# Kernel tuning notes

Hardware: AMD Instinct MI355X
Metric: run time of the kernel (lower is better)

Reference implementation:

```python
import jax, jax.numpy as jnp
import numpy as np

B, T, C, K, V = 4, 4096, 128, 64, 64
EPS = 1e-5


def layer_norm(x, g, b):
    mu = jnp.mean(x, axis=-1, keepdims=True)
    var = jnp.var(x, axis=-1, keepdims=True)
    return (x - mu) * jax.lax.rsqrt(var + EPS) * g + b


def setup_inputs() -> dict:
    key = jax.random.key(0)
    ks = jax.random.split(key, 8)
    s = 1.0 / np.sqrt(C)
    return {
        "x": jax.random.normal(ks[0], (B, T, C), dtype=jnp.float32),
        "Wq": jax.random.uniform(ks[1], (C, K), jnp.float32, -s, s),
        "bq": jnp.zeros((K,), jnp.float32),
        "Wk": jax.random.uniform(ks[2], (C, K), jnp.float32, -s, s),
        "bk": jnp.zeros((K,), jnp.float32),
        "Wv": jax.random.uniform(ks[3], (C, V), jnp.float32, -s, s),
        "bv": jnp.zeros((V,), jnp.float32),
        "gq": jnp.ones((K,), jnp.float32), "bgq": jnp.zeros((K,), jnp.float32),
        "gk": jnp.ones((K,), jnp.float32), "bgk": jnp.zeros((K,), jnp.float32),
        "gv": jnp.ones((V,), jnp.float32), "bgv": jnp.zeros((V,), jnp.float32),
        "go": jnp.ones((V,), jnp.float32), "bgo": jnp.zeros((V,), jnp.float32),
    }


def reference(x, Wq, bq, Wk, bk, Wv, bv, gq, bgq, gk, bgk, gv, bgv, go, bgo):
    # projections: B x T x {K,K,V}
    q = layer_norm(x @ Wq + bq, gq, bgq)
    k = layer_norm(x @ Wk + bk, gk, bgk)
    v = layer_norm(x @ Wv + bv, gv, bgv)
    sqrt_k = jnp.asarray(np.sqrt(K), x.dtype)
    # full B x T x T causal score matrix (faithful to the original bmm+mask)
    logits = jnp.einsum("btk,bsk->bts", q, k) / sqrt_k
    t = jnp.arange(T)
    causal = t[:, None] >= t[None, :]  # lower-triangular incl. diagonal
    logits = jnp.where(causal[None], logits, -jnp.inf)
    probs = jax.nn.softmax(logits, axis=-1)
    read = jnp.einsum("bts,bsv->btv", probs, v)
    read = layer_norm(read, go, bgo)
    return jnp.concatenate([x, read], axis=2)  # B x T x (C+V)
```

## Files before the change

### kernel.cpp

```cpp
#include <hip/hip_runtime.h>

#define TT 4096

typedef unsigned short u16;
typedef unsigned int u32;

typedef short bf16x8 __attribute__((ext_vector_type(8)));
typedef float f32x4 __attribute__((ext_vector_type(4)));

union U8 {
  uint2 q[2];
  uint4 u4;
  bf16x8 v;
  short s[8];
  u32 w[4];
};

static __device__ __forceinline__ u16 f2bf(float f) {
  union { float f; u32 u; } cv;
  cv.f = f;
  u32 r = cv.u + 0x7FFFu + ((cv.u >> 16) & 1u);
  return (u16)(r >> 16);
}
static __device__ __forceinline__ u32 pk2(float a, float b) {
  return (u32)f2bf(a) | ((u32)f2bf(b) << 16);
}
static __device__ __forceinline__ float bf2f(u16 h) {
  union { u32 u; float f; } cv;
  cv.u = ((u32)h) << 16;
  return cv.f;
}
static __device__ __forceinline__ float exp2a(float x) {
  float r; asm("v_exp_f32 %0, %1" : "=v"(r) : "v"(x)); return r;
}
static __device__ __forceinline__ u32 cvtpk(float lo, float hi) {
  u32 r; asm("v_cvt_pk_bf16_f32 %0, %1, %2" : "=v"(r) : "v"(lo), "v"(hi)); return r;
}

__global__ __launch_bounds__(64)
void wpack(const float* __restrict__ Wq, const float* __restrict__ Wk,
           const float* __restrict__ Wv, u16* __restrict__ wf)
{
  const int g = blockIdx.x;
  const int p = g >> 4, s = (g >> 2) & 3, nt = g & 3;
  const int l = threadIdx.x, lg = l >> 4, l15 = l & 15;
  const float* W = (p == 0) ? Wq : (p == 1) ? Wk : Wv;
  const int n = l15 + 16 * nt;
  U8 o;
#pragma unroll
  for (int j = 0; j < 8; ++j) {
    int k = 32 * s + ((j < 4) ? (4 * lg + j) : (16 + 4 * lg + (j - 4)));
    o.s[j] = (short)f2bf(W[k * 64 + n]);
  }
  *(uint4*)(wf + (size_t)(g * 64 + l) * 8) = o.u4;
}

__global__ __launch_bounds__(256)
void proj_mfma(const float* __restrict__ x, const u16* __restrict__ wf,
               const float* __restrict__ bq, const float* __restrict__ bk,
               const float* __restrict__ bv,
               const float* __restrict__ gq, const float* __restrict__ bgq,
               const float* __restrict__ gk, const float* __restrict__ bgk,
               const float* __restrict__ gv, const float* __restrict__ bgv,
               u16* __restrict__ qo, u16* __restrict__ ko, u16* __restrict__ vto,
               float* __restrict__ out)
{
  __shared__ u16 xs[64 * 130];
  const int bx = blockIdx.x;
  const int xcd = bx & 7, i = bx >> 3;
  const int tile = xcd * 32 + (i & 31);
  const int p = i >> 5;
  const int rowbase = tile * 64;
  const int t = threadIdx.x;

  {
    const int row = t >> 2, seg = t & 3;
    const float4* src = (const float4*)(x + (size_t)(rowbase + row) * 128 + seg * 32);
    float4 f[8];
#pragma unroll
    for (int q = 0; q < 8; ++q) f[q] = src[q];
    if ((p == 0 && seg < 2) || (p == 1 && seg >= 2)) {
      float4* dst = (float4*)(out + (size_t)(rowbase + row) * 192 + seg * 32);
#pragma unroll
      for (int q = 0; q < 8; ++q) dst[q] = f[q];
    }
    const int base = row * 256 + seg * 64;
    const int swz = (row & 7) << 4;
    char* xb = (char*)xs;
#pragma unroll
    for (int q = 0; q < 4; ++q) {
      uint4 u;
      u.x = pk2(f[2 * q].x, f[2 * q].y);
      u.y = pk2(f[2 * q].z, f[2 * q].w);
      u.z = pk2(f[2 * q + 1].x, f[2 * q + 1].y);
      u.w = pk2(f[2 * q + 1].z, f[2 * q + 1].w);
      *(uint4*)(xb + ((base + 16 * q) ^ swz)) = u;
    }
  }

  const int w = t >> 6, l = t & 63, lg = l >> 4, l15 = l & 15;
  U8 bfr[4][4];
  const u16* wp = wf + (size_t)p * (16 * 64 * 8);
#pragma unroll
  for (int s = 0; s < 4; ++s)
#pragma unroll
    for (int nt = 0; nt < 4; ++nt)
      bfr[s][nt].u4 = *(const uint4*)(wp + ((s * 4 + nt) * 64 + l) * 8);

  __syncthreads();

  f32x4 acc[4];
#pragma unroll
  for (int nt = 0; nt < 4; ++nt) acc[nt] = (f32x4){0.f, 0.f, 0.f, 0.f};
  const int abase = (16 * w + l15) * 256;
  const int aswz = (l15 & 7) << 4;
  const char* xb = (const char*)xs;
#pragma unroll
  for (int s = 0; s < 4; ++s) {
    U8 af;
    af.q[0] = *(const uint2*)(xb + ((abase + s * 64 + 8 * lg) ^ aswz));
    af.q[1] = *(const uint2*)(xb + ((abase + s * 64 + 8 * lg + 32) ^ aswz));
#pragma unroll
    for (int nt = 0; nt < 4; ++nt)
      acc[nt] = __builtin_amdgcn_mfma_f32_16x16x32_bf16(af.v, bfr[s][nt].v, acc[nt], 0, 0, 0);
  }

  const float* bb = (p == 0) ? bq : (p == 1) ? bk : bv;
  const float* gg = (p == 0) ? gq : (p == 1) ? gk : gv;
  const float* hh = (p == 0) ? bgq : (p == 1) ? bgk : bgv;
  float bcol[4], gcol[4], hcol[4];
#pragma unroll
  for (int nt = 0; nt < 4; ++nt) {
    int col = l15 + 16 * nt;
    bcol[nt] = bb[col]; gcol[nt] = gg[col]; hcol[nt] = hh[col];
  }
  float vals[4][4];
#pragma unroll
  for (int nt = 0; nt < 4; ++nt)
#pragma unroll
    for (int r = 0; r < 4; ++r) vals[nt][r] = acc[nt][r] + bcol[nt];

  float s1[4], s2[4];
#pragma unroll
  for (int r = 0; r < 4; ++r) {
    s1[r] = vals[0][r] + vals[1][r] + vals[2][r] + vals[3][r];
    s2[r] = vals[0][r] * vals[0][r] + vals[1][r] * vals[1][r]
          + vals[2][r] * vals[2][r] + vals[3][r] * vals[3][r];
#pragma unroll
    for (int d = 1; d < 16; d <<= 1) {
      s1[r] += __shfl_xor(s1[r], d);
      s2[r] += __shfl_xor(s2[r], d);
    }
  }

  if (p < 2) {
    u16* dst = (p == 0) ? qo : ko;
#pragma unroll
    for (int r = 0; r < 4; ++r) {
      float mu = s1[r] * (1.f / 64.f);
      float var = s2[r] * (1.f / 64.f) - mu * mu;
      float rs = rsqrtf(var + 1e-5f);
      int grow = rowbase + 16 * w + 4 * lg + r;
#pragma unroll
      for (int nt = 0; nt < 4; ++nt)
        dst[(size_t)grow * 64 + l15 + 16 * nt] =
            f2bf((vals[nt][r] - mu) * rs * gcol[nt] + hcol[nt]);
    }
  } else {
    u16* vls = xs;
    __syncthreads();
#pragma unroll
    for (int r = 0; r < 4; ++r) {
      float mu = s1[r] * (1.f / 64.f);
      float var = s2[r] * (1.f / 64.f) - mu * mu;
      float rs = rsqrtf(var + 1e-5f);
      int row = 16 * w + 4 * lg + r;
#pragma unroll
      for (int nt = 0; nt < 4; ++nt)
        vls[row * 65 + l15 + 16 * nt] =
            f2bf((vals[nt][r] - mu) * rs * gcol[nt] + hcol[nt]);
    }
    __syncthreads();
    const int b = rowbase >> 12;
    const int tl = rowbase & 4095;
    const int col = t >> 2;
    const int tq = (t & 3) * 16;
    U8 o0, o1;
#pragma unroll
    for (int i = 0; i < 8; ++i) o0.s[i] = (short)vls[(tq + i) * 65 + col];
#pragma unroll
    for (int i = 0; i < 8; ++i) o1.s[i] = (short)vls[(tq + 8 + i) * 65 + col];
    u16* dst = vto + (size_t)(b * 64 + col) * TT + tl + tq;
    *(uint4*)(dst + 0) = o0.u4;
    *(uint4*)(dst + 8) = o1.u4;
  }
}

__global__ __launch_bounds__(256)
void attn_pair4n(const u16* __restrict__ qg, const u16* __restrict__ kg,
                 const u16* __restrict__ vtg,
                 float* __restrict__ lP, u16* __restrict__ aP)
{
  __shared__ u16 kl4[4 * 64 * 64];
  __shared__ u16 vl4[4 * 64 * 64];
  const int bx = blockIdx.x;
  const int xcd = bx & 7, b = xcd >> 1, e2 = xcd & 1;
  const int j = e2 * 136 + (bx >> 3);
  int M = 0;
  while ((M + 1) * (M + 2) <= j) ++M;
  const int ip = j - M * (M + 1);
  const int e = (ip >= M + 1) ? 1 : 0;
  const int s = ip - e * (M + 1);
  const int pr = 2 * M + e;
  const int qa = 2 * pr, qb = 2 * pr + 1;
  const int it0 = 4 * s;
  const int it1 = min(it0 + 4, qb + 1);

  const int t = threadIdx.x;
  const int w = t >> 6, l = t & 63;
  const int l15 = l & 15, lg = l >> 4;
  const int swzl = (l15 & 7) << 4;

  const int wbaseA = qa * 64 + 16 * w, wbaseB = qb * 64 + 16 * w;
  const int qrowA = wbaseA + l15, qrowB = wbaseB + l15;
  const u16* qrpA = qg + (size_t)(b * TT + qrowA) * 64;
  const u16* qrpB = qg + (size_t)(b * TT + qrowB) * 64;
  U8 qfA[2], qfB[2];
#pragma unroll
  for (int hh = 0; hh < 2; ++hh) {
    qfA[hh].q[0] = *(const uint2*)(qrpA + 32 * hh + 4 * lg);
    qfA[hh].q[1] = *(const uint2*)(qrpA + 32 * hh + 4 * lg + 16);
    qfB[hh].q[0] = *(const uint2*)(qrpB + 32 * hh + 4 * lg);
    qfB[hh].q[1] = *(const uint2*)(qrpB + 32 * hh + 4 * lg + 16);
  }

  {
    const int key = t >> 2, part = t & 3;
    const int sbase = key * 128 + part * 32;
    const int ssw = (key & 7) << 4;
    uint4 kr[4][2], vr[4][2];
#pragma unroll
    for (int tt = 0; tt < 4; ++tt) {
      int tile = it0 + tt; if (tile >= it1) tile = it1 - 1;
      const u16* ks = kg + (size_t)(b * TT + tile * 64 + key) * 64 + part * 16;
      kr[tt][0] = ((const uint4*)ks)[0];
      kr[tt][1] = ((const uint4*)ks)[1];
      const u16* vs = vtg + (size_t)(b * 64 + key) * TT + tile * 64 + part * 16;
      vr[tt][0] = ((const uint4*)vs)[0];
      vr[tt][1] = ((const uint4*)vs)[1];
    }
#pragma unroll
    for (int tt = 0; tt < 4; ++tt) {
      char* kd = (char*)kl4 + tt * 8192;
      char* vd = (char*)vl4 + tt * 8192;
      *(uint4*)(kd + ((sbase + 0) ^ ssw)) = kr[tt][0];
      *(uint4*)(kd + ((sbase + 16) ^ ssw)) = kr[tt][1];
      *(uint4*)(vd + ((sbase + 0) ^ ssw)) = vr[tt][0];
      *(uint4*)(vd + ((sbase + 16) ^ ssw)) = vr[tt][1];
    }
  }
  __syncthreads();

  const float C = 0.18033688011112042f;
  float lA = 0.f, lB = 0.f;
  f32x4 accA[4], accB[4];
#pragma unroll
  for (int ct = 0; ct < 4; ++ct) {
    accA[ct] = (f32x4){0.f, 0.f, 0.f, 0.f};
    accB[ct] = (f32x4){0.f, 0.f, 0.f, 0.f};
  }

  int toff = 0;
  for (int it = it0; it < it1; ++it, toff += 8192) {
    const int kb = it * 64;
    const char* kp = (const char*)kl4 + toff;
    const char* vp = (const char*)vl4 + toff;

    f32x4 stA[4], stB[4];
    __builtin_amdgcn_s_setprio(1);
#pragma unroll
    for (int t4 = 0; t4 < 4; ++t4) {
      const int rbase = (16 * t4 + l15) * 128 + 8 * lg;
      U8 kf0, kf1;
      kf0.q[0] = *(const uint2*)(kp + ((rbase + 0) ^ swzl));
      kf0.q[1] = *(const uint2*)(kp + ((rbase + 32) ^ swzl));
      kf1.q[0] = *(const uint2*)(kp + ((rbase + 64) ^ swzl));
      kf1.q[1] = *(const uint2*)(kp + ((rbase + 96) ^ swzl));
      f32x4 dA = {0.f, 0.f, 0.f, 0.f};
      dA = __builtin_amdgcn_mfma_f32_16x16x32_bf16(kf0.v, qfA[0].v, dA, 0, 0, 0);
      dA = __builtin_amdgcn_mfma_f32_16x16x32_bf16(kf1.v, qfA[1].v, dA, 0, 0, 0);
      stA[t4] = dA;
      f32x4 dB = {0.f, 0.f, 0.f, 0.f};
      dB = __builtin_amdgcn_mfma_f32_16x16x32_bf16(kf0.v, qfB[0].v, dB, 0, 0, 0);
      dB = __builtin_amdgcn_mfma_f32_16x16x32_bf16(kf1.v, qfB[1].v, dB, 0, 0, 0);
      stB[t4] = dB;
    }
    __builtin_amdgcn_s_setprio(0);

    float pA[16], pB[16];
    const bool maskA = (kb + 63 > wbaseA);
    if (maskA) {
#pragma unroll
      for (int t4 = 0; t4 < 4; ++t4) {
#pragma unroll
        for (int r = 0; r < 4; ++r) {
          int keyidx = kb + 16 * t4 + 4 * lg + r;
          float e = exp2a(stA[t4][r] * C);
          pA[t4 * 4 + r] = (keyidx > qrowA) ? 0.f : e;
        }
      }
    } else {
#pragma unroll
      for (int t4 = 0; t4 < 4; ++t4) {
#pragma unroll
        for (int r = 0; r < 4; ++r) pA[t4 * 4 + r] = exp2a(stA[t4][r] * C);
      }
    }
    const bool maskB = (kb + 63 > wbaseB);
    if (maskB) {
#pragma unroll
      for (int t4 = 0; t4 < 4; ++t4) {
#pragma unroll
        for (int r = 0; r < 4; ++r) {
          int keyidx = kb + 16 * t4 + 4 * lg + r;
          float e = exp2a(stB[t4][r] * C);
          pB[t4 * 4 + r] = (keyidx > qrowB) ? 0.f : e;
        }
      }
    } else {
#pragma unroll
      for (int t4 = 0; t4 < 4; ++t4) {
#pragma unroll
        for (int r = 0; r < 4; ++r) pB[t4 * 4 + r] = exp2a(stB[t4][r] * C);
      }
    }
    float smA[8], smB[8];
#pragma unroll
    for (int i = 0; i < 8; ++i) {
      smA[i] = pA[2 * i] + pA[2 * i + 1];
      smB[i] = pB[2 * i] + pB[2 * i + 1];
    }
#pragma unroll
    for (int i = 0; i < 4; ++i) {
      smA[i] = smA[2 * i] + smA[2 * i + 1];
      smB[i] = smB[2 * i] + smB[2 * i + 1];
    }
    float rsA = (smA[0] + smA[1]) + (smA[2] + smA[3]);
    float rsB = (smB[0] + smB[1]) + (smB[2] + smB[3]);
    rsA += __shfl_xor(rsA, 16);
    rsB += __shfl_xor(rsB, 16);
    rsA += __shfl_xor(rsA, 32);
    rsB += __shfl_xor(rsB, 32);
    lA += rsA;
    lB += rsB;

    U8 paA[2], paB[2];
#pragma unroll
    for (int u = 0; u < 2; ++u) {
#pragma unroll
      for (int k2 = 0; k2 < 4; ++k2) {
        paA[u].w[k2] = cvtpk(pA[8 * u + 2 * k2], pA[8 * u + 2 * k2 + 1]);
        paB[u].w[k2] = cvtpk(pB[8 * u + 2 * k2], pB[8 * u + 2 * k2 + 1]);
      }
    }

    __builtin_amdgcn_s_setprio(1);
#pragma unroll
    for (int ct = 0; ct < 4; ++ct) {
      const int vb = (16 * ct + l15) * 128 + 8 * lg;
#pragma unroll
      for (int u = 0; u < 2; ++u) {
        U8 vf;
        vf.q[0] = *(const uint2*)(vp + ((vb + 64 * u + 0) ^ swzl));
        vf.q[1] = *(const uint2*)(vp + ((vb + 64 * u + 32) ^ swzl));
        accA[ct] = __builtin_amdgcn_mfma_f32_16x16x32_bf16(paA[u].v, vf.v, accA[ct], 0, 0, 0);
        accB[ct] = __builtin_amdgcn_mfma_f32_16x16x32_bf16(paB[u].v, vf.v, accB[ct], 0, 0, 0);
      }
    }
    __builtin_amdgcn_s_setprio(0);
  }

  const int jqA = 2 * M * (M + 1) + (2 * e) * (M + 1) + s;
  const int jqB = 2 * M * (M + 1) + (2 * e + 1) * (M + 1) + s;
  const size_t pbA = (size_t)(b * 544 + jqA) * 64;
  const size_t pbB = (size_t)(b * 544 + jqB) * 64;
  if (lg == 0) {
    lP[pbA + 16 * w + l15] = lA;
    lP[pbB + 16 * w + l15] = lB;
  }
#pragma unroll
  for (int ct = 0; ct < 4; ++ct) {
#pragma unroll
    for (int r = 0; r < 4; ++r) {
      int rin = 16 * w + 4 * lg + r;
      aP[(pbA + rin) * 64 + l15 + 16 * ct] = f2bf(accA[ct][r]);
      aP[(pbB + rin) * 64 + l15 + 16 * ct] = f2bf(accB[ct][r]);
    }
  }
}

__global__ __launch_bounds__(256)
void attn_merge4n(const float* __restrict__ lP, const u16* __restrict__ aP,
                  const float* __restrict__ go, const float* __restrict__ bgo,
                  float* __restrict__ out)
{
  const int t = threadIdx.x;
  const int w = t >> 6, c = t & 63;
  const int row = blockIdx.x * 4 + w;
  const int tid2 = row >> 6, rin = row & 63;
  const int b = tid2 >> 6, q = tid2 & 63;
  const int Q = q >> 2;
  const int base_q = b * 544 + 2 * Q * (Q + 1) + (q & 3) * (Q + 1);
  const int ns = Q + 1;

  float L = 0.f, o = 0.f;
  for (int s = 0; s < ns; ++s) {
    const size_t pb = (size_t)(base_q + s) * 64;
    L += lP[pb + rin];
    o += bf2f(aP[(pb + rin) * 64 + c]);
  }
  o /= L;

  float s1 = o, s2 = o * o;
#pragma unroll
  for (int d = 1; d < 64; d <<= 1) {
    s1 += __shfl_xor(s1, d);
    s2 += __shfl_xor(s2, d);
  }
  float mu = s1 * (1.f / 64.f);
  float var = s2 * (1.f / 64.f) - mu * mu;
  float rs = rsqrtf(var + 1e-5f);
  out[(size_t)row * 192 + 128 + c] = (o - mu) * rs * go[c] + bgo[c];
}

__global__ __launch_bounds__(128)
void attn1(const u16* __restrict__ qg, const u16* __restrict__ kg,
           const u16* __restrict__ vtg,
           const float* __restrict__ go, const float* __restrict__ bgo,
           float* __restrict__ out)
{
  __shared__ u16 kl[64 * 64];
  __shared__ u16 vl[64 * 64];
  const int bx = blockIdx.x;
  const int tt = (bx < 256) ? bx : (767 - bx);
  const int b = tt >> 7;
  const int q0 = (tt & 127) * 32;
  const int tid = threadIdx.x;
  const int w = tid >> 6;
  const int l = tid & 63;
  const int l15 = l & 15;
  const int lg = l >> 4;
  const int swzl = (l15 & 7) << 4;

  const int qrow = q0 + 16 * w + l15;
  const u16* qrp = qg + (size_t)(b * TT + qrow) * 64;
  U8 qf[2];
#pragma unroll
  for (int h = 0; h < 2; ++h) {
    qf[h].q[0] = *(const uint2*)(qrp + 32 * h + 4 * lg);
    qf[h].q[1] = *(const uint2*)(qrp + 32 * h + 4 * lg + 16);
  }

  float m_run = -1e30f, l_run = 0.f;
  f32x4 acc[4];
#pragma unroll
  for (int ct = 0; ct < 4; ++ct) acc[ct] = (f32x4){0.f, 0.f, 0.f, 0.f};

  const int nkv = (q0 >> 6) + 1;
  for (int it = 0; it < nkv; ++it) {
    const int kb = it * 64;
    {
      const int key = tid >> 1;
      const int dh = (tid & 1) * 32;
      const u16* ks = kg + (size_t)(b * TT + kb + key) * 64 + dh;
      uint4 d0 = *(const uint4*)(ks + 0);
      uint4 d1 = *(const uint4*)(ks + 8);
      uint4 d2 = *(const uint4*)(ks + 16);
      uint4 d3 = *(const uint4*)(ks + 24);
      const int base = key * 128 + dh * 2;
      const int sw = (key & 7) << 4;
      char* kd = (char*)kl;
      *(uint4*)(kd + ((base + 0) ^ sw)) = d0;
      *(uint4*)(kd + ((base + 16) ^ sw)) = d1;
      *(uint4*)(kd + ((base + 32) ^ sw)) = d2;
      *(uint4*)(kd + ((base + 48) ^ sw)) = d3;
      const u16* vs = vtg + (size_t)(b * 64 + key) * TT + kb + dh;
      uint4 e0 = *(const uint4*)(vs + 0);
      uint4 e1 = *(const uint4*)(vs + 8);
      uint4 e2 = *(const uint4*)(vs + 16);
      uint4 e3 = *(const uint4*)(vs + 24);
      char* vd = (char*)vl;
      *(uint4*)(vd + ((base + 0) ^ sw)) = e0;
      *(uint4*)(vd + ((base + 16) ^ sw)) = e1;
      *(uint4*)(vd + ((base + 32) ^ sw)) = e2;
      *(uint4*)(vd + ((base + 48) ^ sw)) = e3;
    }
    __syncthreads();

    f32x4 st[4];
#pragma unroll
    for (int t4 = 0; t4 < 4; ++t4) {
      const int rbase = (16 * t4 + l15) * 128 + 8 * lg;
      const char* kp = (const char*)kl;
      U8 kf0, kf1;
      kf0.q[0] = *(const uint2*)(kp + ((rbase + 0) ^ swzl));
      kf0.q[1] = *(const uint2*)(kp + ((rbase + 32) ^ swzl));
      kf1.q[0] = *(const uint2*)(kp + ((rbase + 64) ^ swzl));
      kf1.q[1] = *(const uint2*)(kp + ((rbase + 96) ^ swzl));
      f32x4 d = {0.f, 0.f, 0.f, 0.f};
      d = __builtin_amdgcn_mfma_f32_16x16x32_bf16(kf0.v, qf[0].v, d, 0, 0, 0);
      d = __builtin_amdgcn_mfma_f32_16x16x32_bf16(kf1.v, qf[1].v, d, 0, 0, 0);
      st[t4] = d;
    }

    float sv[16];
    const bool needmask = (kb + 63 > q0 + 16 * w);
#pragma unroll
    for (int t4 = 0; t4 < 4; ++t4) {
#pragma unroll
      for (int r = 0; r < 4; ++r) {
        float sc = st[t4][r] * 0.125f;
        if (needmask) {
          int keyidx = kb + 16 * t4 + 4 * lg + r;
          if (keyidx > qrow) sc = -1e30f;
        }
        sv[t4 * 4 + r] = sc;
      }
    }
    float mt = sv[0];
#pragma unroll
    for (int i = 1; i < 16; ++i) mt = fmaxf(mt, sv[i]);
    mt = fmaxf(mt, __shfl_xor(mt, 16));
    mt = fmaxf(mt, __shfl_xor(mt, 32));
    const float mnew = fmaxf(m_run, mt);
    const float al = __expf(m_run - mnew);
    float p[16];
    float rsum = 0.f;
#pragma unroll
    for (int i = 0; i < 16; ++i) { p[i] = __expf(sv[i] - mnew); rsum += p[i]; }
    rsum += __shfl_xor(rsum, 16);
    rsum += __shfl_xor(rsum, 32);
    l_run = l_run * al + rsum;
    m_run = mnew;
    float ar[4];
#pragma unroll
    for (int r = 0; r < 4; ++r) ar[r] = __shfl(al, 4 * lg + r);
#pragma unroll
    for (int ct = 0; ct < 4; ++ct) {
#pragma unroll
      for (int r = 0; r < 4; ++r) acc[ct][r] *= ar[r];
    }
    U8 pa[2];
#pragma unroll
    for (int u = 0; u < 2; ++u) {
#pragma unroll
      for (int i = 0; i < 8; ++i) pa[u].s[i] = (short)f2bf(p[8 * u + i]);
    }

#pragma unroll
    for (int ct = 0; ct < 4; ++ct) {
      const int vb = (16 * ct + l15) * 128 + 8 * lg;
      const char* vp = (const char*)vl;
#pragma unroll
      for (int u = 0; u < 2; ++u) {
        U8 vf;
        vf.q[0] = *(const uint2*)(vp + ((vb + 64 * u + 0) ^ swzl));
        vf.q[1] = *(const uint2*)(vp + ((vb + 64 * u + 32) ^ swzl));
        acc[ct] = __builtin_amdgcn_mfma_f32_16x16x32_bf16(pa[u].v, vf.v, acc[ct], 0, 0, 0);
      }
    }
    __syncthreads();
  }

  float linv[4];
#pragma unroll
  for (int r = 0; r < 4; ++r) linv[r] = 1.f / __shfl(l_run, 4 * lg + r);
  float o[4][4];
#pragma unroll
  for (int ct = 0; ct < 4; ++ct) {
#pragma unroll
    for (int r = 0; r < 4; ++r) o[ct][r] = acc[ct][r] * linv[r];
  }
  float s1[4], s2[4];
#pragma unroll
  for (int r = 0; r < 4; ++r) {
    s1[r] = o[0][r] + o[1][r] + o[2][r] + o[3][r];
    s2[r] = o[0][r] * o[0][r] + o[1][r] * o[1][r] + o[2][r] * o[2][r] + o[3][r] * o[3][r];
#pragma unroll
    for (int d = 1; d < 16; d <<= 1) {
      s1[r] += __shfl_xor(s1[r], d);
      s2[r] += __shfl_xor(s2[r], d);
    }
  }
  float gov[4], bgv2[4];
#pragma unroll
  for (int ct = 0; ct < 4; ++ct) {
    gov[ct] = go[16 * ct + l15];
    bgv2[ct] = bgo[16 * ct + l15];
  }
#pragma unroll
  for (int r = 0; r < 4; ++r) {
    float mu = s1[r] * (1.f / 64.f);
    float var = s2[r] * (1.f / 64.f) - mu * mu;
    float rs = rsqrtf(var + 1e-5f);
    int row = q0 + 16 * w + 4 * lg + r;
    float* op = out + (size_t)(b * TT + row) * 192 + 128;
#pragma unroll
    for (int ct = 0; ct < 4; ++ct)
      op[16 * ct + l15] = (o[ct][r] - mu) * rs * gov[ct] + bgv2[ct];
  }
}

extern "C" void kernel_launch(void* const* d_in, const int* in_sizes, int n_in,
                              void* d_out, int out_size, void* d_ws, size_t ws_size,
                              hipStream_t stream) {
  (void)in_sizes; (void)n_in; (void)out_size;
  const float* x   = (const float*)d_in[0];
  const float* Wq  = (const float*)d_in[1];
  const float* bq  = (const float*)d_in[2];
  const float* Wk  = (const float*)d_in[3];
  const float* bk  = (const float*)d_in[4];
  const float* Wv  = (const float*)d_in[5];
  const float* bv  = (const float*)d_in[6];
  const float* gq  = (const float*)d_in[7];
  const float* bgq = (const float*)d_in[8];
  const float* gk  = (const float*)d_in[9];
  const float* bgk = (const float*)d_in[10];
  const float* gv  = (const float*)d_in[11];
  const float* bgv = (const float*)d_in[12];
  const float* go  = (const float*)d_in[13];
  const float* bgo = (const float*)d_in[14];
  float* out = (float*)d_out;

  char* wsb = (char*)d_ws;
  u16* qws  = (u16*)wsb;
  u16* kws  = (u16*)(wsb + (2u << 20));
  u16* vtws = (u16*)(wsb + (4u << 20));
  u16* wfr  = (u16*)(wsb + (6u << 20));
  const size_t OFF_LP = (6u << 20) + 65536;

  wpack<<<48, 64, 0, stream>>>(Wq, Wk, Wv, wfr);
  proj_mfma<<<768, 256, 0, stream>>>(x, wfr, bq, bk, bv,
                                     gq, bgq, gk, bgk, gv, bgv,
                                     qws, kws, vtws, out);

  {
    const size_t SEG4 = 4u * 544;
    const size_t LPS = SEG4 * 64 * 4;
    const size_t APS = SEG4 * 64 * 64 * 2;
    const size_t OFF_AP = OFF_LP + LPS;
    const size_t NEED = OFF_AP + APS;

    if (ws_size >= NEED) {
      float* lP = (float*)(wsb + OFF_LP);
      u16*   aP = (u16*)(wsb + OFF_AP);
      attn_pair4n<<<1088, 256, 0, stream>>>(qws, kws, vtws, lP, aP);
      attn_merge4n<<<4096, 256, 0, stream>>>(lP, aP, go, bgo, out);
    } else {
      attn1<<<512, 128, 0, stream>>>(qws, kws, vtws, go, bgo, out);
    }
  }
}
```

Before: 59.02 us.

## Reduce split-K attention partials with float atomics instead of a merge pass

Rather than writing bf16 per-segment partial outputs and row sums to a buffer and summing them in a merge kernel, the attention kernel now atomically adds fp32 partials into a per-row accumulator, which is zeroed by a memset first. The final kernel only divides and applies the output layer norm. The aim is to cut partial-buffer traffic and the merge loop's reads. The cost is heavy global atomic contention, about 16 float atomics per thread per block, plus an extra memset launch. The reduction order also becomes nondeterministic.

```diff
diff --git a/kernel.cpp b/kernel.cpp
--- a/kernel.cpp
+++ b/kernel.cpp
@@ -24,11 +24,6 @@
 }
 static __device__ __forceinline__ u32 pk2(float a, float b) {
   return (u32)f2bf(a) | ((u32)f2bf(b) << 16);
-}
-static __device__ __forceinline__ float bf2f(u16 h) {
-  union { u32 u; float f; } cv;
-  cv.u = ((u32)h) << 16;
-  return cv.f;
 }
 static __device__ __forceinline__ float exp2a(float x) {
   float r; asm("v_exp_f32 %0, %1" : "=v"(r) : "v"(x)); return r;
@@ -197,9 +192,9 @@
 }
 
 __global__ __launch_bounds__(256)
-void attn_pair4n(const u16* __restrict__ qg, const u16* __restrict__ kg,
+void attn_pair4a(const u16* __restrict__ qg, const u16* __restrict__ kg,
                  const u16* __restrict__ vtg,
-                 float* __restrict__ lP, u16* __restrict__ aP)
+                 float* __restrict__ oSum, float* __restrict__ lSum)
 {
   __shared__ u16 kl4[4 * 64 * 64];
   __shared__ u16 vl4[4 * 64 * 64];
@@ -380,46 +375,30 @@
     __builtin_amdgcn_s_setprio(0);
   }
 
-  const int jqA = 2 * M * (M + 1) + (2 * e) * (M + 1) + s;
-  const int jqB = 2 * M * (M + 1) + (2 * e + 1) * (M + 1) + s;
-  const size_t pbA = (size_t)(b * 544 + jqA) * 64;
-  const size_t pbB = (size_t)(b * 544 + jqB) * 64;
   if (lg == 0) {
-    lP[pbA + 16 * w + l15] = lA;
-    lP[pbB + 16 * w + l15] = lB;
+    atomicAdd(&lSum[b * TT + wbaseA + l15], lA);
+    atomicAdd(&lSum[b * TT + wbaseB + l15], lB);
   }
 #pragma unroll
   for (int ct = 0; ct < 4; ++ct) {
 #pragma unroll
     for (int r = 0; r < 4; ++r) {
       int rin = 16 * w + 4 * lg + r;
-      aP[(pbA + rin) * 64 + l15 + 16 * ct] = f2bf(accA[ct][r]);
-      aP[(pbB + rin) * 64 + l15 + 16 * ct] = f2bf(accB[ct][r]);
+      atomicAdd(&oSum[((size_t)(b * TT + qa * 64 + rin)) * 64 + l15 + 16 * ct], accA[ct][r]);
+      atomicAdd(&oSum[((size_t)(b * TT + qb * 64 + rin)) * 64 + l15 + 16 * ct], accB[ct][r]);
     }
   }
 }
 
 __global__ __launch_bounds__(256)
-void attn_merge4n(const float* __restrict__ lP, const u16* __restrict__ aP,
-                  const float* __restrict__ go, const float* __restrict__ bgo,
-                  float* __restrict__ out)
+void attn_lnfin(const float* __restrict__ oSum, const float* __restrict__ lSum,
+                const float* __restrict__ go, const float* __restrict__ bgo,
+                float* __restrict__ out)
 {
   const int t = threadIdx.x;
   const int w = t >> 6, c = t & 63;
   const int row = blockIdx.x * 4 + w;
-  const int tid2 = row >> 6, rin = row & 63;
-  const int b = tid2 >> 6, q = tid2 & 63;
-  const int Q = q >> 2;
-  const int base_q = b * 544 + 2 * Q * (Q + 1) + (q & 3) * (Q + 1);
-  const int ns = Q + 1;
-
-  float L = 0.f, o = 0.f;
-  for (int s = 0; s < ns; ++s) {
-    const size_t pb = (size_t)(base_q + s) * 64;
-    L += lP[pb + rin];
-    o += bf2f(aP[(pb + rin) * 64 + c]);
-  }
-  o /= L;
+  float o = oSum[(size_t)row * 64 + c] / lSum[row];
 
   float s1 = o, s2 = o * o;
 #pragma unroll
@@ -637,27 +616,23 @@
   u16* kws  = (u16*)(wsb + (2u << 20));
   u16* vtws = (u16*)(wsb + (4u << 20));
   u16* wfr  = (u16*)(wsb + (6u << 20));
-  const size_t OFF_LP = (6u << 20) + 65536;
+  const size_t OFF_OS = (6u << 20) + 65536;
+  const size_t OSZ = (size_t)4 * TT * 64 * 4;
+  const size_t LSZ = (size_t)4 * TT * 4;
+  const size_t NEED = OFF_OS + OSZ + LSZ;
+  float* oSum = (float*)(wsb + OFF_OS);
+  float* lSum = (float*)(wsb + OFF_OS + OSZ);
 
   wpack<<<48, 64, 0, stream>>>(Wq, Wk, Wv, wfr);
   proj_mfma<<<768, 256, 0, stream>>>(x, wfr, bq, bk, bv,
                                      gq, bgq, gk, bgk, gv, bgv,
                                      qws, kws, vtws, out);
 
-  {
-    const size_t SEG4 = 4u * 544;
-    const size_t LPS = SEG4 * 64 * 4;
-    const size_t APS = SEG4 * 64 * 64 * 2;
-    const size_t OFF_AP = OFF_LP + LPS;
-    const size_t NEED = OFF_AP + APS;
-
-    if (ws_size >= NEED) {
-      float* lP = (float*)(wsb + OFF_LP);
-      u16*   aP = (u16*)(wsb + OFF_AP);
-      attn_pair4n<<<1088, 256, 0, stream>>>(qws, kws, vtws, lP, aP);
-      attn_merge4n<<<4096, 256, 0, stream>>>(lP, aP, go, bgo, out);
-    } else {
-      attn1<<<512, 128, 0, stream>>>(qws, kws, vtws, go, bgo, out);
-    }
-  }
-}
+  if (ws_size >= NEED) {
+    hipMemsetAsync(wsb + OFF_OS, 0, OSZ + LSZ, stream);
+    attn_pair4a<<<1088, 256, 0, stream>>>(qws, kws, vtws, oSum, lSum);
+    attn_lnfin<<<4096, 256, 0, stream>>>(oSum, lSum, go, bgo, out);
+  } else {
+    attn1<<<512, 128, 0, stream>>>(qws, kws, vtws, go, bgo, out);
+  }
+}
```

Result: slower. 68.89 us (+16.7%).
